# Optimization experiments

Measured on AMD Instinct MI355X. Metric: run time of the kernel, lower is better.

The kernel has to match this reference:

```python
import jax, jax.numpy as jnp
import numpy as np

LAMBDA_K_TAU = 0.1
RIDGE = 0.1


def _masked_cov(x, mask, counts):
    """Covariance of masked rows. x: [B,S,D], mask: [B,S] float, counts: [B] float.
    Equivalent to packing the masked rows (batch_2d_tensor) then _torch_cov."""
    xm = x * mask[..., None]
    mean = xm.sum(axis=1) / counts[:, None]                 # [B,D]
    xc = (xm - mean[:, None, :]) * mask[..., None]          # [B,S,D]
    cov = jnp.einsum('bsi,bsj->bij', xc, xc)
    return cov / (counts - 1.0)[:, None, None]


def _calc_label_cov_inv(task_cov, label_cov):
    d = task_cov.shape[-1]
    eye = jnp.eye(d, dtype=task_cov.dtype)
    return jnp.linalg.inv(LAMBDA_K_TAU * label_cov + (1.0 - LAMBDA_K_TAU) * task_cov + RIDGE * eye)


def setup_inputs() -> dict:
    key = jax.random.key(0)
    ks = jax.random.split(key, 6)
    B, S, Q, D = 256, 512, 256, 512
    support_set = jax.random.normal(ks[0], (B, S, D), dtype=jnp.float32)
    support_labels = jax.random.randint(ks[1], (B, S), 0, 2, dtype=jnp.int32)
    query_set = jax.random.normal(ks[2], (B, Q, D), dtype=jnp.float32)
    # lengths in [len//2, len] so both classes are present and counts > 1
    support_set_lengths = jax.random.randint(ks[3], (B,), S // 2, S + 1, dtype=jnp.int32)
    query_set_lengths = jax.random.randint(ks[4], (B,), Q // 2, Q + 1, dtype=jnp.int32)
    log_prediction_scaling = jnp.asarray(np.log(10.0), dtype=jnp.float32)
    return {
        'support_set': support_set,
        'support_labels': support_labels,
        'query_set': query_set,
        'support_set_lengths': support_set_lengths,
        'query_set_lengths': query_set_lengths,
        'log_prediction_scaling': log_prediction_scaling,
    }


def reference(support_set, support_labels, query_set, support_set_lengths,
              query_set_lengths, log_prediction_scaling):
    B, S, D = support_set.shape
    Q = query_set.shape[1]
    f32 = support_set.dtype

    sup_valid = (jnp.arange(S)[None, :] < support_set_lengths[:, None]).astype(f32)  # [B,S]
    mask_pos = (support_labels == 1).astype(f32) * sup_valid                          # [B,S]
    mask_neg = (support_labels == 0).astype(f32) * sup_valid

    pos_counts = mask_pos.sum(axis=1)   # [B]
    neg_counts = mask_neg.sum(axis=1)
    sup_counts = support_set_lengths.astype(f32)

    positive_mean = jnp.einsum('bsd,bs->bd', support_set, mask_pos) / pos_counts[:, None]
    negative_mean = jnp.einsum('bsd,bs->bd', support_set, mask_neg) / neg_counts[:, None]

    cov_mats = _masked_cov(support_set, sup_valid, sup_counts)   # task covariance
    pos_mats = _masked_cov(support_set, mask_pos, pos_counts)    # == cov of packed positives
    neg_mats = _masked_cov(support_set, mask_neg, neg_counts)

    pos_inv = _calc_label_cov_inv(cov_mats, pos_mats)  # [B,D,D]
    neg_inv = _calc_label_cov_inv(cov_mats, neg_mats)

    q_valid = (jnp.arange(Q)[None, :] < query_set_lengths[:, None]).astype(f32)  # [B,Q]

    pos_diff = positive_mean[:, None, :] - query_set  # [B,Q,D]
    neg_diff = negative_mean[:, None, :] - query_set
    pos_maha = jnp.einsum('bik,bkx,bix->bi', pos_diff, pos_inv, pos_diff) * q_valid
    neg_maha = jnp.einsum('bik,bkx,bix->bi', neg_diff, neg_inv, neg_diff) * q_valid

    logit_scale = jnp.exp(log_prediction_scaling)
    # scale is applied inside batch_calculate_mahalanobis_logits AND again in forward
    logits = jnp.stack([neg_maha, pos_maha], axis=-1) * (-1.0) * logit_scale
    return logits * logit_scale  # [B,Q,2]
```

## Files before the change

kernel.cpp:

```cpp
#include <hip/hip_runtime.h>
#include <hip/hip_bf16.h>

#define TPB 256
constexpr int B_ = 256, S_ = 512, D_ = 512, Q_ = 256, NM_ = 512;
constexpr int NB = 64, NT = 8;

typedef _Float16 f16x8 __attribute__((ext_vector_type(8)));
typedef float f32x4 __attribute__((ext_vector_type(4)));

__device__ __forceinline__ int pidx(int j, int a){ return j*(15-j)/2 + (a-j-1); }

__device__ __forceinline__ void decode_mt(int bid, int W, int& m, int& t){
  int x = bid & 7, r = bid >> 3;
  t = r % W; int u = r / W;
  m = (((u >> 1)*8 + x) << 1) | (u & 1);
}

__device__ __forceinline__ void stage_D(const float* __restrict__ src, size_t ld,
                                        float (*dst)[68], int t)
{
  int r = t >> 2, seg = (t & 3) * 16;
  const float4* s4 = (const float4*)(src + (size_t)r*ld + seg);
  #pragma unroll
  for (int i=0;i<4;i++) *((float4*)&dst[r][seg + i*4]) = s4[i];
}

__device__ __forceinline__ void mm_acc68(const float (*Aop)[68], const float (*Bop)[68],
                                         float acc[4][4], int tr, int tc)
{
  for (int kk=0;kk<64;kk++){
    float4 av = *((const float4*)&Aop[kk][tr*4]);
    float4 bv = *((const float4*)&Bop[kk][tc*4]);
    float a[4]={av.x,av.y,av.z,av.w}, b2[4]={bv.x,bv.y,bv.z,bv.w};
    #pragma unroll
    for (int u=0;u<4;u++)
      #pragma unroll
      for (int v=0;v<4;v++) acc[u][v] = fmaf(a[u], b2[v], acc[u][v]);
  }
}

__global__ __launch_bounds__(TPB) void k_prep(const float* __restrict__ X,
                                              const int* __restrict__ labels,
                                              const int* __restrict__ slen,
                                              unsigned short* __restrict__ Xvh,
                                              unsigned short* __restrict__ Xvl,
                                              float* __restrict__ mu,
                                              float* __restrict__ cnt,
                                              unsigned int* __restrict__ wpbits)
{
  int b = blockIdx.y, dz = blockIdx.x;
  int d0 = dz*64;
  int t = threadIdx.x;
  __shared__ float Tl[64][65];
  __shared__ int lab[S_];
  __shared__ float red[TPB];
  int L = slen[b];
  for (int s = t; s < S_; s += TPB){
    int lb = labels[b*S_ + s];
    lab[s] = (s < L) ? lb : -1;
  }
  __syncthreads();
  if (dz == 0 && t < 16){
    unsigned int wword = 0;
    for (int i2=0;i2<32;i2++) if (lab[t*32+i2]==1) wword |= (1u<<i2);
    wpbits[b*16+t] = wword;
  }
  int cpi=0, cni=0;
  for (int s=t; s<S_; s+=TPB){ cpi += (lab[s]==1); cni += (lab[s]==0); }
  red[t] = (float)cpi; __syncthreads();
  for (int o=TPB/2;o>0;o>>=1){ if(t<o) red[t]+=red[t+o]; __syncthreads(); }
  float cp = red[0]; __syncthreads();
  red[t] = (float)cni; __syncthreads();
  for (int o=TPB/2;o>0;o>>=1){ if(t<o) red[t]+=red[t+o]; __syncthreads(); }
  float cn = red[0];
  if (dz==0 && t==0){ cnt[b*2+0]=cn; cnt[b*2+1]=cp; }
  __syncthreads();

  int dr = t>>2, sc = (t&3)*16;
  float accp = 0.f, accn = 0.f;
  for (int sz=0; sz<8; sz++){
    int s0 = sz*64;
    const float* src = X + ((size_t)b*S_ + s0)*D_ + d0;
    { int r = t>>2, seg = (t&3)*16;
      const float4* s4 = (const float4*)(src + (size_t)r*D_ + seg);
      #pragma unroll
      for (int i=0;i<4;i++){ float4 v = s4[i];
        Tl[seg+i*4+0][r]=v.x; Tl[seg+i*4+1][r]=v.y; Tl[seg+i*4+2][r]=v.z; Tl[seg+i*4+3][r]=v.w; } }
    __syncthreads();
    union U16 { unsigned short u[8]; uint4 v; };
    U16 H[2], Lo[2];
    #pragma unroll
    for (int g=0; g<2; g++)
      #pragma unroll
      for (int i=0;i<8;i++){
        int si = sc + g*8 + i;
        float x = (s0+si < L) ? Tl[dr][si] : 0.f;
        _Float16 hh = (_Float16)x;
        float lo = x - (float)hh;
        H[g].u[i]  = __builtin_bit_cast(unsigned short, hh);
        Lo[g].u[i] = __builtin_bit_cast(unsigned short, (_Float16)lo);
      }
    size_t o = ((size_t)b*D_ + d0+dr)*S_ + s0 + sc;
    *(uint4*)(Xvh+o)   = H[0].v;  *(uint4*)(Xvh+o+8) = H[1].v;
    *(uint4*)(Xvl+o)   = Lo[0].v; *(uint4*)(Xvl+o+8) = Lo[1].v;
    #pragma unroll
    for (int i=0;i<16;i++){
      int si = sc + i;
      int e = lab[s0+si];
      float x = Tl[dr][si];
      accp += (e==1) ? x : 0.f;
      accn += (e==0) ? x : 0.f;
    }
    __syncthreads();
  }
  accp += __shfl_xor(accp, 1, 64);
  accp += __shfl_xor(accp, 2, 64);
  accn += __shfl_xor(accn, 1, 64);
  accn += __shfl_xor(accn, 2, 64);
  if ((t&3)==0){
    int d = d0 + dr;
    float stv = (float)L;
    float* mb = mu + (size_t)b*3*D_;
    mb[0*D_ + d] = accn/cn;
    mb[1*D_ + d] = accp/cp;
    mb[2*D_ + d] = (accn+accp)/stv;
  }
}

__global__ __launch_bounds__(TPB,2) void k_gram(const unsigned short* __restrict__ Xvh,
                                                const unsigned short* __restrict__ Xvl,
                                                const unsigned int* __restrict__ wpbits,
                                                const float* __restrict__ mu,
                                                const float* __restrict__ cnt,
                                                const int* __restrict__ slen,
                                                float* __restrict__ A)
{
  __shared__ unsigned short sAvh[128][32], sAvl[128][32], sAph[128][32], sApl[128][32],
                            sBvh[128][32], sBvl[128][32];
  int id = blockIdx.x;
  int g = id>>3;
  int b = (g/10)*8 + (id&7);
  int z = g%10;
  int ti=0; while (z >= 4-ti){ z -= 4-ti; ti++; } int tj = ti + z;
  int i0 = ti*128, j0 = tj*128;
  int t = threadIdx.x, lane = t&63, w = t>>6;
  int wr = w>>1, wc = w&1, l15 = lane&15;

  f32x4 acc_t[4][4], acc_p[4][4];
  f32x4 z4 = {0.f,0.f,0.f,0.f};
  #pragma unroll
  for (int mf=0;mf<4;mf++)
    #pragma unroll
    for (int nf=0;nf<4;nf++){ acc_t[mf][nf]=z4; acc_p[mf][nf]=z4; }

  const size_t baseA = ((size_t)b*D_ + i0)*S_;
  const size_t baseB = ((size_t)b*D_ + j0)*S_;
  int phx = (lane>>4) ^ ((l15>>1)&3);

  for (int ks=0; ks<16; ks++){
    int s0 = ks*32;
    unsigned int wpw = wpbits[b*16 + ks];
    __syncthreads();
    #pragma unroll
    for (int h=0; h<2; h++){
      int ci = t + h*256;
      int row = ci>>2, cpos = ci&3;
      int ph = cpos ^ ((row>>1)&3);
      size_t ga = baseA + (size_t)row*S_ + s0 + cpos*8;
      size_t gb = baseB + (size_t)row*S_ + s0 + cpos*8;
      uint4 vh = *(const uint4*)(Xvh+ga);
      uint4 vl = *(const uint4*)(Xvl+ga);
      uint4 bh = *(const uint4*)(Xvh+gb);
      uint4 bl = *(const uint4*)(Xvl+gb);
      unsigned int m8 = (wpw >> (cpos*8)) & 0xFFu;
      uint4 mk;
      mk.x = ((m8&1u)?0xFFFFu:0u)  | ((m8&2u)?0xFFFF0000u:0u);
      mk.y = ((m8&4u)?0xFFFFu:0u)  | ((m8&8u)?0xFFFF0000u:0u);
      mk.z = ((m8&16u)?0xFFFFu:0u) | ((m8&32u)?0xFFFF0000u:0u);
      mk.w = ((m8&64u)?0xFFFFu:0u) | ((m8&128u)?0xFFFF0000u:0u);
      uint4 p4, q4;
      p4.x = vh.x&mk.x; p4.y = vh.y&mk.y; p4.z = vh.z&mk.z; p4.w = vh.w&mk.w;
      q4.x = vl.x&mk.x; q4.y = vl.y&mk.y; q4.z = vl.z&mk.z; q4.w = vl.w&mk.w;
      *(uint4*)&sAvh[row][ph*8] = vh;
      *(uint4*)&sAvl[row][ph*8] = vl;
      *(uint4*)&sAph[row][ph*8] = p4;
      *(uint4*)&sApl[row][ph*8] = q4;
      *(uint4*)&sBvh[row][ph*8] = bh;
      *(uint4*)&sBvl[row][ph*8] = bl;
    }
    __syncthreads();
    f16x8 Avh[4], Avl[4], Aph[4], Apl[4];
    #pragma unroll
    for (int mf=0;mf<4;mf++){
      int r = wr*64 + mf*16 + l15;
      Avh[mf] = __builtin_bit_cast(f16x8, *(const uint4*)&sAvh[r][phx*8]);
      Avl[mf] = __builtin_bit_cast(f16x8, *(const uint4*)&sAvl[r][phx*8]);
      Aph[mf] = __builtin_bit_cast(f16x8, *(const uint4*)&sAph[r][phx*8]);
      Apl[mf] = __builtin_bit_cast(f16x8, *(const uint4*)&sApl[r][phx*8]);
    }
    #pragma unroll
    for (int nf=0;nf<4;nf++){
      int r = wc*64 + nf*16 + l15;
      f16x8 Bh = __builtin_bit_cast(f16x8, *(const uint4*)&sBvh[r][phx*8]);
      f16x8 Bl = __builtin_bit_cast(f16x8, *(const uint4*)&sBvl[r][phx*8]);
      #pragma unroll
      for (int mf=0;mf<4;mf++){
        acc_t[mf][nf] = __builtin_amdgcn_mfma_f32_16x16x32_f16(Avh[mf], Bh, acc_t[mf][nf],0,0,0);
        acc_t[mf][nf] = __builtin_amdgcn_mfma_f32_16x16x32_f16(Avh[mf], Bl, acc_t[mf][nf],0,0,0);
        acc_t[mf][nf] = __builtin_amdgcn_mfma_f32_16x16x32_f16(Avl[mf], Bh, acc_t[mf][nf],0,0,0);
        acc_p[mf][nf] = __builtin_amdgcn_mfma_f32_16x16x32_f16(Aph[mf], Bh, acc_p[mf][nf],0,0,0);
        acc_p[mf][nf] = __builtin_amdgcn_mfma_f32_16x16x32_f16(Aph[mf], Bl, acc_p[mf][nf],0,0,0);
        acc_p[mf][nf] = __builtin_amdgcn_mfma_f32_16x16x32_f16(Apl[mf], Bh, acc_p[mf][nf],0,0,0);
      }
    }
  }
  float cn = cnt[b*2+0], cp = cnt[b*2+1];
  float stv = (float)slen[b];
  float kn = 0.1f/(cn-1.f), kp = 0.1f/(cp-1.f), kt = 0.9f/(stv-1.f);
  float rn = 0.1f*cn/(cn-1.f), rp = 0.1f*cp/(cp-1.f), rt = 0.9f*stv/(stv-1.f);
  const float* mb = mu + (size_t)b*3*D_;
  float* A0 = A + (size_t)(b*2+0)*D_*D_;
  float* A1 = A + (size_t)(b*2+1)*D_*D_;
  int rbase = i0 + wr*64 + (lane>>4)*4;
  int cbase = j0 + wc*64 + l15;
  #pragma unroll
  for (int mf=0;mf<4;mf++){
    #pragma unroll
    for (int i=0;i<4;i++){
      int r = rbase + mf*16 + i;
      float mnr = mb[r], mpr = mb[D_+r], mtr = mb[2*D_+r];
      #pragma unroll
      for (int nf=0;nf<4;nf++){
        int c = cbase + nf*16;
        float mnc = mb[c], mpc = mb[D_+c], mtc = mb[2*D_+c];
        float gp = acc_p[mf][nf][i];
        float gt = acc_t[mf][nf][i];
        float gn = gt - gp;
        float diag = (r==c)?0.1f:0.f;
        A0[(size_t)r*D_ + c] = kn*gn + kt*gt - rn*mnr*mnc - rt*mtr*mtc + diag;
        A1[(size_t)r*D_ + c] = kp*gp + kt*gt - rp*mpr*mpc - rt*mtr*mtc + diag;
      }
    }
  }
}

__global__ __launch_bounds__(TPB) void k_diag(float* __restrict__ A,
                                              float* __restrict__ invDT, int j)
{
  int m, t0; decode_mt(blockIdx.x, 1, m, t0); (void)t0;
  int t = threadIdx.x;
  __shared__ float Ld[64][65];
  __shared__ float Iv[64][65];
  float* Ab = A + (size_t)m*D_*D_ + (size_t)(j*NB)*D_ + j*NB;
  for (int l=t; l<4096; l+=TPB){ int r=l>>6, c=l&63; Ld[r][c] = Ab[(size_t)r*D_ + c]; Iv[r][c] = 0.f; }
  __syncthreads();
  for (int k=0;k<64;k++){
    if (t==0) Ld[k][k] = sqrtf(Ld[k][k]);
    __syncthreads();
    if (t>k && t<64) Ld[t][k] /= Ld[k][k];
    __syncthreads();
    for (int l=t; l<4096; l+=TPB){
      int r=l>>6, c=l&63;
      if (r>k && c>k) Ld[r][c] = fmaf(-Ld[r][k], Ld[c][k], Ld[r][c]);
    }
    __syncthreads();
  }
  if (t < 64){
    int c = t;
    Iv[c][c] = 1.f/Ld[c][c];
    for (int r=c+1;r<64;r++){
      float s = 0.f;
      for (int k2=c;k2<r;k2++) s += Ld[r][k2]*Iv[k2][c];
      Iv[r][c] = -s/Ld[r][r];
    }
  }
  __syncthreads();
  float* Ib = invDT + ((size_t)m*8 + j)*4096;
  for (int l=t; l<4096; l+=TPB){ Ib[l] = Iv[l&63][l>>6]; }
}

__global__ __launch_bounds__(TPB) void k_panel(float* __restrict__ A,
                                               const float* __restrict__ invDT,
                                               unsigned short* __restrict__ Ut,
                                               int j, int W)
{
  int m, ti; decode_mt(blockIdx.x, W, m, ti);
  int ib = j + 1 + ti;
  int t = threadIdx.x, tr = t&15, tc = t>>4;
  __shared__ float Ta[64][68], Tb[64][68];
  float* U = A + (size_t)m*D_*D_ + (size_t)(j*NB)*D_ + ib*NB;
  stage_D(invDT + ((size_t)m*8 + j)*4096, 64, Ta, t);
  stage_D(U, D_, Tb, t);
  __syncthreads();
  float acc[4][4] = {};
  mm_acc68(Ta, Tb, acc, tr, tc);
  #pragma unroll
  for (int u=0;u<4;u++){
    float4 o = make_float4(acc[u][0],acc[u][1],acc[u][2],acc[u][3]);
    *((float4*)(U + (size_t)(tr*4+u)*D_ + tc*4)) = o;
  }
  __syncthreads();
  unsigned short* shh = (unsigned short*)Ta;
  unsigned short* shl = (unsigned short*)Tb;
  #pragma unroll
  for (int u=0;u<4;u++)
    #pragma unroll
    for (int v=0;v<4;v++){
      float val = acc[u][v];
      _Float16 h = (_Float16)val;
      float lo = val - (float)h;
      shh[(tc*4+v)*72 + tr*4+u] = __builtin_bit_cast(unsigned short, h);
      shl[(tc*4+v)*72 + tr*4+u] = __builtin_bit_cast(unsigned short, (_Float16)lo);
    }
  __syncthreads();
  unsigned short* Ub = Ut + ((size_t)m*28 + pidx(j, ib)) * 8192;
  { int r = t>>2, cs = (t&3)*16;
    *(uint4*)(Ub + r*64 + cs)          = *(uint4*)&shh[r*72 + cs];
    *(uint4*)(Ub + r*64 + cs + 8)      = *(uint4*)&shh[r*72 + cs + 8];
    *(uint4*)(Ub + 4096 + r*64 + cs)   = *(uint4*)&shl[r*72 + cs];
    *(uint4*)(Ub + 4096 + r*64 + cs+8) = *(uint4*)&shl[r*72 + cs + 8];
  }
}

__device__ __forceinline__ void trail_stage(const unsigned short* __restrict__ Ua,
                                            const unsigned short* __restrict__ Ub,
                                            unsigned short (*Ah)[72], unsigned short (*Al)[72],
                                            unsigned short (*Bh)[72], unsigned short (*Bl)[72],
                                            int t)
{
  int r = t>>2, cs = (t&3)*16;
  *(uint4*)&Ah[r][cs]   = *(const uint4*)(Ua + r*64 + cs);
  *(uint4*)&Ah[r][cs+8] = *(const uint4*)(Ua + r*64 + cs + 8);
  *(uint4*)&Al[r][cs]   = *(const uint4*)(Ua + 4096 + r*64 + cs);
  *(uint4*)&Al[r][cs+8] = *(const uint4*)(Ua + 4096 + r*64 + cs + 8);
  *(uint4*)&Bh[r][cs]   = *(const uint4*)(Ub + r*64 + cs);
  *(uint4*)&Bh[r][cs+8] = *(const uint4*)(Ub + r*64 + cs + 8);
  *(uint4*)&Bl[r][cs]   = *(const uint4*)(Ub + 4096 + r*64 + cs);
  *(uint4*)&Bl[r][cs+8] = *(const uint4*)(Ub + 4096 + r*64 + cs + 8);
}

__device__ __forceinline__ void trail_mfma(const unsigned short (*Ah)[72], const unsigned short (*Al)[72],
                                           const unsigned short (*Bh)[72], const unsigned short (*Bl)[72],
                                           f32x4 acc[4], int w, int l15, int lk)
{
  #pragma unroll
  for (int s=0;s<2;s++){
    f16x8 Afh = __builtin_bit_cast(f16x8, *(const uint4*)&Ah[w*16 + l15][s*32 + lk*8]);
    f16x8 Afl = __builtin_bit_cast(f16x8, *(const uint4*)&Al[w*16 + l15][s*32 + lk*8]);
    #pragma unroll
    for (int ni=0;ni<4;ni++){
      f16x8 Bfh = __builtin_bit_cast(f16x8, *(const uint4*)&Bh[ni*16 + l15][s*32 + lk*8]);
      f16x8 Bfl = __builtin_bit_cast(f16x8, *(const uint4*)&Bl[ni*16 + l15][s*32 + lk*8]);
      acc[ni] = __builtin_amdgcn_mfma_f32_16x16x32_f16(Afh, Bfh, acc[ni],0,0,0);
      acc[ni] = __builtin_amdgcn_mfma_f32_16x16x32_f16(Afh, Bfl, acc[ni],0,0,0);
      acc[ni] = __builtin_amdgcn_mfma_f32_16x16x32_f16(Afl, Bfh, acc[ni],0,0,0);
    }
  }
}

__device__ __forceinline__ void trail_rmw(float* __restrict__ Cb, const f32x4 acc[4],
                                          int w, int l15, int lk)
{
  #pragma unroll
  for (int ni=0;ni<4;ni++)
    #pragma unroll
    for (int i=0;i<4;i++){
      int r = w*16 + lk*4 + i, cc = ni*16 + l15;
      float* pC = Cb + (size_t)r*D_ + cc;
      *pC -= acc[ni][i];
    }
}

__global__ __launch_bounds__(TPB) void k_trailrow(float* __restrict__ A,
                                                  const unsigned short* __restrict__ Ut,
                                                  int j, int row, int W)
{
  int m, z; decode_mt(blockIdx.x, W, m, z);
  int b2 = row + z;
  int t = threadIdx.x, lane = t&63, w = t>>6, l15 = lane&15, lk = lane>>4;
  __shared__ unsigned short Ah[64][72], Al[64][72], Bh[64][72], Bl[64][72];
  const unsigned short* Um = Ut + (size_t)m*28*8192;
  trail_stage(Um + (size_t)pidx(j,row)*8192, Um + (size_t)pidx(j,b2)*8192, Ah, Al, Bh, Bl, t);
  __syncthreads();
  f32x4 acc[4];
  #pragma unroll
  for (int ni=0;ni<4;ni++) acc[ni] = (f32x4){0.f,0.f,0.f,0.f};
  trail_mfma(Ah, Al, Bh, Bl, acc, w, l15, lk);
  float* Cb = A + (size_t)m*D_*D_ + (size_t)(row*NB)*D_ + b2*NB;
  trail_rmw(Cb, acc, w, l15, lk);
}

__global__ __launch_bounds__(TPB) void k_trail2(float* __restrict__ A,
                                                const unsigned short* __restrict__ Ut,
                                                int jb, int W)
{
  int m, z; decode_mt(blockIdx.x, W, m, z);
  int base = jb + 2;
  int Tn = NT - base;
  int p = 0, zz = z;
  while (zz >= Tn - p){ zz -= Tn - p; p++; }
  int a2 = base + p, b2 = a2 + zz;
  int t = threadIdx.x, lane = t&63, w = t>>6, l15 = lane&15, lk = lane>>4;
  __shared__ unsigned short Ah[64][72], Al[64][72], Bh[64][72], Bl[64][72];
  const unsigned short* Um = Ut + (size_t)m*28*8192;
  f32x4 acc[4];
  #pragma unroll
  for (int ni=0;ni<4;ni++) acc[ni] = (f32x4){0.f,0.f,0.f,0.f};
  #pragma unroll
  for (int c=0;c<2;c++){
    int j = jb + c;
    __syncthreads();
    trail_stage(Um + (size_t)pidx(j,a2)*8192, Um + (size_t)pidx(j,b2)*8192, Ah, Al, Bh, Bl, t);
    __syncthreads();
    trail_mfma(Ah, Al, Bh, Bl, acc, w, l15, lk);
  }
  float* Cb = A + (size_t)m*D_*D_ + (size_t)(a2*NB)*D_ + b2*NB;
  trail_rmw(Cb, acc, w, l15, lk);
}

__global__ __launch_bounds__(TPB) void k_solvefin(const float* __restrict__ Qs,
                                                  const float* __restrict__ mu,
                                                  const float* __restrict__ A,
                                                  const float* __restrict__ invDT,
                                                  float* __restrict__ Z,
                                                  const int* __restrict__ qlen,
                                                  const float* __restrict__ lps,
                                                  float* __restrict__ out)
{
  int m, t0; decode_mt(blockIdx.x, 4, m, t0);
  int q0 = t0*NB;
  int b = m>>1, cls = m&1;
  int t = threadIdx.x, tr = t&15, tc = t>>4;
  __shared__ float Ta[64][68], Tb[64][68];
  const float* Am = A + (size_t)m*D_*D_;
  float* Zm = Z + (size_t)m*D_*Q_;
  const float* muv = mu + ((size_t)b*3 + cls)*D_;
  float cs[4] = {0.f,0.f,0.f,0.f};
  for (int j=0;j<NT;j++){
    float acc[4][4];
    {
      float4 mv = *(const float4*)&muv[j*NB + tr*4];
      #pragma unroll
      for (int v=0;v<4;v++){
        float4 qv = *(const float4*)&Qs[((size_t)b*Q_ + q0 + tc*4 + v)*D_ + j*NB + tr*4];
        acc[0][v] = mv.x - qv.x;
        acc[1][v] = mv.y - qv.y;
        acc[2][v] = mv.z - qv.z;
        acc[3][v] = mv.w - qv.w;
      }
    }
    for (int k=0;k<j;k++){
      stage_D(Am + (size_t)(k*NB)*D_ + j*NB, D_, Ta, t);
      { int r = t >> 2, seg = (t & 3)*16;
        const float4* s4 = (const float4*)(Zm + (size_t)(k*NB + r)*Q_ + q0 + seg);
        #pragma unroll
        for (int i=0;i<4;i++) *((float4*)&Tb[r][seg + i*4]) = s4[i];
      }
      __syncthreads();
      for (int kk=0;kk<64;kk++){
        float4 av = *((const float4*)&Ta[kk][tr*4]);
        float4 bv = *((const float4*)&Tb[kk][tc*4]);
        float a[4]={av.x,av.y,av.z,av.w}, bb2[4]={bv.x,bv.y,bv.z,bv.w};
        #pragma unroll
        for (int u=0;u<4;u++)
          #pragma unroll
          for (int v=0;v<4;v++) acc[u][v] = fmaf(-a[u], bb2[v], acc[u][v]);
      }
      __syncthreads();
    }
    #pragma unroll
    for (int u=0;u<4;u++){
      int cb = (tc*4) ^ ((tr&7)<<2);
      *((float4*)&Tb[tr*4+u][cb]) = make_float4(acc[u][0],acc[u][1],acc[u][2],acc[u][3]);
    }
    stage_D(invDT + ((size_t)m*8 + j)*4096, 64, Ta, t);
    __syncthreads();
    float o4[4][4] = {};
    for (int kk=0;kk<64;kk++){
      float4 av = *((const float4*)&Ta[kk][tr*4]);
      float4 bv = *((const float4*)&Tb[kk][(tc*4) ^ (((kk>>2)&7)<<2)]);
      float a[4]={av.x,av.y,av.z,av.w}, bb2[4]={bv.x,bv.y,bv.z,bv.w};
      #pragma unroll
      for (int u=0;u<4;u++)
        #pragma unroll
        for (int v=0;v<4;v++) o4[u][v] = fmaf(a[u], bb2[v], o4[u][v]);
    }
    if (j < NT-1){
      #pragma unroll
      for (int u=0;u<4;u++){
        float4 o = make_float4(o4[u][0], o4[u][1], o4[u][2], o4[u][3]);
        *((float4*)(Zm + (size_t)(j*NB + tr*4+u)*Q_ + q0 + tc*4)) = o;
      }
    }
    #pragma unroll
    for (int u=0;u<4;u++)
      #pragma unroll
      for (int v=0;v<4;v++) cs[v] = fmaf(o4[u][v], o4[u][v], cs[v]);
    __syncthreads();
  }
  float* red = &Ta[0][0];
  #pragma unroll
  for (int v=0;v<4;v++) red[(tc*4+v)*16 + tr] = cs[v];
  __syncthreads();
  if (t < 64){
    float s = 0.f;
    #pragma unroll
    for (int i=0;i<16;i++) s += red[t*16 + i];
    int q = q0 + t;
    float valid = (q < qlen[b]) ? 1.f : 0.f;
    float s2 = expf(2.f*lps[0]);
    out[((size_t)b*Q_ + q)*2 + cls] = -s2*s*valid;
  }
}

extern "C" void kernel_launch(void* const* d_in, const int* in_sizes, int n_in,
                              void* d_out, int out_size, void* d_ws, size_t ws_size,
                              hipStream_t stream) {
  (void)in_sizes; (void)n_in; (void)out_size;
  const float* X   = (const float*)d_in[0];
  const int*   lab = (const int*)d_in[1];
  const float* Qs  = (const float*)d_in[2];
  const int*   sl  = (const int*)d_in[3];
  const int*   ql  = (const int*)d_in[4];
  const float* lps = (const float*)d_in[5];
  float* out = (float*)d_out;

  float* A  = (float*)d_ws;
  float* Z  = A + (size_t)NM_*D_*D_;
  unsigned short* Xvh = (unsigned short*)Z;
  unsigned short* Xvl = Xvh + (size_t)B_*D_*S_;
  unsigned short* Ut  = (unsigned short*)Z;
  float* invDT = Z + (size_t)NM_*D_*Q_;
  float* mu   = invDT + (size_t)NM_*8*64*64;
  float* cnt  = mu + (size_t)B_*3*D_;
  unsigned int* wpbits = (unsigned int*)(cnt + B_*2);
  size_t need = (size_t)((char*)(wpbits + B_*16) - (char*)d_ws);
  if (ws_size < need) return;

  k_prep<<<dim3(8, B_), dim3(TPB), 0, stream>>>(X, lab, sl, Xvh, Xvl, mu, cnt, wpbits);
  k_gram<<<dim3(2560), dim3(TPB), 0, stream>>>(Xvh, Xvl, wpbits, mu, cnt, sl, A);

  for (int j=0; j<NT; j+=2){
    k_diag<<<dim3(NM_), dim3(TPB), 0, stream>>>(A, invDT, j);
    int nb0 = NT-1-j;
    if (nb0 > 0){
      k_panel<<<dim3(NM_*nb0), dim3(TPB), 0, stream>>>(A, invDT, Ut, j, nb0);
      int wr = NT - (j+1);
      k_trailrow<<<dim3(NM_*wr), dim3(TPB), 0, stream>>>(A, Ut, j, j+1, wr);
      k_diag<<<dim3(NM_), dim3(TPB), 0, stream>>>(A, invDT, j+1);
      int nb1 = NT-1-(j+1);
      if (nb1 > 0){
        k_panel<<<dim3(NM_*nb1), dim3(TPB), 0, stream>>>(A, invDT, Ut, j+1, nb1);
        int Tn = NT - (j+2);
        int np = Tn*(Tn+1)/2;
        if (np > 0) k_trail2<<<dim3(NM_*np), dim3(TPB), 0, stream>>>(A, Ut, j, np);
      }
    }
  }

  k_solvefin<<<dim3(NM_*4), dim3(TPB), 0, stream>>>(Qs, mu, A, invDT, Z, ql, lps, out);
}
```

Baseline: 2.392 ms.

## Assign one row strip per block in trailing update to reuse A panel tiles

The double-column trailing update now gives each block a full row strip of tiles instead of a single tile. The strip's A-side panel tiles for both columns are staged once into shared memory and reused across all column tiles in the strip, which cuts global loads and block count. The cost is fewer blocks (less parallelism), strips of uneven length that cause load imbalance, and twice the shared memory per block, which can lower occupancy.

Measured after the change: 2.428 ms. Within noise of the previous version (+1.5%).

```diff
diff --git a/kernel.cpp b/kernel.cpp
--- a/kernel.cpp
+++ b/kernel.cpp
@@ -322,21 +322,15 @@
   }
 }
 
-__device__ __forceinline__ void trail_stage(const unsigned short* __restrict__ Ua,
-                                            const unsigned short* __restrict__ Ub,
-                                            unsigned short (*Ah)[72], unsigned short (*Al)[72],
-                                            unsigned short (*Bh)[72], unsigned short (*Bl)[72],
-                                            int t)
+__device__ __forceinline__ void stage_pair(const unsigned short* __restrict__ U,
+                                           unsigned short (*Xh)[72], unsigned short (*Xl)[72],
+                                           int t)
 {
   int r = t>>2, cs = (t&3)*16;
-  *(uint4*)&Ah[r][cs]   = *(const uint4*)(Ua + r*64 + cs);
-  *(uint4*)&Ah[r][cs+8] = *(const uint4*)(Ua + r*64 + cs + 8);
-  *(uint4*)&Al[r][cs]   = *(const uint4*)(Ua + 4096 + r*64 + cs);
-  *(uint4*)&Al[r][cs+8] = *(const uint4*)(Ua + 4096 + r*64 + cs + 8);
-  *(uint4*)&Bh[r][cs]   = *(const uint4*)(Ub + r*64 + cs);
-  *(uint4*)&Bh[r][cs+8] = *(const uint4*)(Ub + r*64 + cs + 8);
-  *(uint4*)&Bl[r][cs]   = *(const uint4*)(Ub + 4096 + r*64 + cs);
-  *(uint4*)&Bl[r][cs+8] = *(const uint4*)(Ub + 4096 + r*64 + cs + 8);
+  *(uint4*)&Xh[r][cs]   = *(const uint4*)(U + r*64 + cs);
+  *(uint4*)&Xh[r][cs+8] = *(const uint4*)(U + r*64 + cs + 8);
+  *(uint4*)&Xl[r][cs]   = *(const uint4*)(U + 4096 + r*64 + cs);
+  *(uint4*)&Xl[r][cs+8] = *(const uint4*)(U + 4096 + r*64 + cs + 8);
 }
 
 __device__ __forceinline__ void trail_mfma(const unsigned short (*Ah)[72], const unsigned short (*Al)[72],
@@ -380,7 +374,8 @@
   int t = threadIdx.x, lane = t&63, w = t>>6, l15 = lane&15, lk = lane>>4;
   __shared__ unsigned short Ah[64][72], Al[64][72], Bh[64][72], Bl[64][72];
   const unsigned short* Um = Ut + (size_t)m*28*8192;
-  trail_stage(Um + (size_t)pidx(j,row)*8192, Um + (size_t)pidx(j,b2)*8192, Ah, Al, Bh, Bl, t);
+  stage_pair(Um + (size_t)pidx(j,row)*8192, Ah, Al, t);
+  stage_pair(Um + (size_t)pidx(j,b2)*8192, Bh, Bl, t);
   __syncthreads();
   f32x4 acc[4];
   #pragma unroll
@@ -390,32 +385,38 @@
   trail_rmw(Cb, acc, w, l15, lk);
 }
 
-__global__ __launch_bounds__(TPB) void k_trail2(float* __restrict__ A,
-                                                const unsigned short* __restrict__ Ut,
-                                                int jb, int W)
-{
-  int m, z; decode_mt(blockIdx.x, W, m, z);
-  int base = jb + 2;
-  int Tn = NT - base;
-  int p = 0, zz = z;
-  while (zz >= Tn - p){ zz -= Tn - p; p++; }
-  int a2 = base + p, b2 = a2 + zz;
+__global__ __launch_bounds__(TPB) void k_trail2_s(float* __restrict__ A,
+                                                  const unsigned short* __restrict__ Ut,
+                                                  int jb, int W)
+{
+  int m, strip; decode_mt(blockIdx.x, W, m, strip);
+  int a2 = jb + 2 + strip;
   int t = threadIdx.x, lane = t&63, w = t>>6, l15 = lane&15, lk = lane>>4;
-  __shared__ unsigned short Ah[64][72], Al[64][72], Bh[64][72], Bl[64][72];
+  __shared__ unsigned short sb[8*64*72];
+  unsigned short (*A0h)[72] = (unsigned short(*)[72])(sb + 0*64*72);
+  unsigned short (*A0l)[72] = (unsigned short(*)[72])(sb + 1*64*72);
+  unsigned short (*A1h)[72] = (unsigned short(*)[72])(sb + 2*64*72);
+  unsigned short (*A1l)[72] = (unsigned short(*)[72])(sb + 3*64*72);
+  unsigned short (*B0h)[72] = (unsigned short(*)[72])(sb + 4*64*72);
+  unsigned short (*B0l)[72] = (unsigned short(*)[72])(sb + 5*64*72);
+  unsigned short (*B1h)[72] = (unsigned short(*)[72])(sb + 6*64*72);
+  unsigned short (*B1l)[72] = (unsigned short(*)[72])(sb + 7*64*72);
   const unsigned short* Um = Ut + (size_t)m*28*8192;
-  f32x4 acc[4];
-  #pragma unroll
-  for (int ni=0;ni<4;ni++) acc[ni] = (f32x4){0.f,0.f,0.f,0.f};
-  #pragma unroll
-  for (int c=0;c<2;c++){
-    int j = jb + c;
-    __syncthreads();
-    trail_stage(Um + (size_t)pidx(j,a2)*8192, Um + (size_t)pidx(j,b2)*8192, Ah, Al, Bh, Bl, t);
-    __syncthreads();
-    trail_mfma(Ah, Al, Bh, Bl, acc, w, l15, lk);
-  }
-  float* Cb = A + (size_t)m*D_*D_ + (size_t)(a2*NB)*D_ + b2*NB;
-  trail_rmw(Cb, acc, w, l15, lk);
+  float* Am = A + (size_t)m*D_*D_;
+  stage_pair(Um + (size_t)pidx(jb,   a2)*8192, A0h, A0l, t);
+  stage_pair(Um + (size_t)pidx(jb+1, a2)*8192, A1h, A1l, t);
+  for (int b2 = a2; b2 < NT; b2++){
+    if (b2 > a2) __syncthreads();
+    stage_pair(Um + (size_t)pidx(jb,   b2)*8192, B0h, B0l, t);
+    stage_pair(Um + (size_t)pidx(jb+1, b2)*8192, B1h, B1l, t);
+    __syncthreads();
+    f32x4 acc[4];
+    #pragma unroll
+    for (int ni=0;ni<4;ni++) acc[ni] = (f32x4){0.f,0.f,0.f,0.f};
+    trail_mfma(A0h, A0l, B0h, B0l, acc, w, l15, lk);
+    trail_mfma(A1h, A1l, B1h, B1l, acc, w, l15, lk);
+    trail_rmw(Am + (size_t)(a2*NB)*D_ + b2*NB, acc, w, l15, lk);
+  }
 }
 
 __global__ __launch_bounds__(TPB) void k_solvefin(const float* __restrict__ Qs,
@@ -551,9 +552,8 @@
       int nb1 = NT-1-(j+1);
       if (nb1 > 0){
         k_panel<<<dim3(NM_*nb1), dim3(TPB), 0, stream>>>(A, invDT, Ut, j+1, nb1);
-        int Tn = NT - (j+2);
-        int np = Tn*(Tn+1)/2;
-        if (np > 0) k_trail2<<<dim3(NM_*np), dim3(TPB), 0, stream>>>(A, Ut, j, np);
+        int nstr = NT - (j+2);
+        if (nstr > 0) k_trail2_s<<<dim3(NM_*nstr), dim3(TPB), 0, stream>>>(A, Ut, j, nstr);
       }
     }
   }
```
